# Kernel optimization log

Hardware: AMD Instinct MI355X
Metric: run time of the kernel (lower is better)

The kernel has to match this reference:

```python
import jax, jax.numpy as jnp
import numpy as np

N_NODES = 50000
N_EDGES = 640000
D = 128


def _sage_conv(x, src, dst, W_l, b, W_r, n_nodes):
    # PyG SAGEConv with mean aggregation:
    #   out = lin_l(mean_{j in N(i)} x_j) + lin_r(x_i)
    msg = x[src]                                              # [E, D] gather
    agg = jax.ops.segment_sum(msg, dst, num_segments=n_nodes)  # [N, D] scatter-add
    cnt = jax.ops.segment_sum(jnp.ones((src.shape[0], 1), x.dtype), dst,
                              num_segments=n_nodes)            # [N, 1]
    agg = agg / jnp.maximum(cnt, 1.0)                          # mean (0 if no neighbors)
    return agg @ W_l + b + x @ W_r


def setup_inputs() -> dict:
    key = jax.random.key(0)
    ks = jax.random.split(key, 8)
    s = 1.0 / np.sqrt(D)
    x = jax.random.normal(ks[0], (N_NODES, D), dtype=jnp.float32)
    edge_index = jax.random.randint(ks[1], (2, N_EDGES), 0, N_NODES, dtype=jnp.int64)
    return {
        "x": x,
        "edge_index": edge_index,
        "W_l1": jax.random.normal(ks[2], (D, D), dtype=jnp.float32) * s,
        "b1": jnp.zeros((D,), jnp.float32),
        "W_r1": jax.random.normal(ks[3], (D, D), dtype=jnp.float32) * s,
        "W_l2": jax.random.normal(ks[4], (D, D), dtype=jnp.float32) * s,
        "b2": jnp.zeros((D,), jnp.float32),
        "W_r2": jax.random.normal(ks[5], (D, D), dtype=jnp.float32) * s,
        "W_l3": jax.random.normal(ks[6], (D, D), dtype=jnp.float32) * s,
        "b3": jnp.zeros((D,), jnp.float32),
        "W_r3": jax.random.normal(ks[7], (D, D), dtype=jnp.float32) * s,
    }


def reference(x, edge_index, W_l1, b1, W_r1, W_l2, b2, W_r2, W_l3, b3, W_r3):
    src, dst = edge_index[0], edge_index[1]
    n = x.shape[0]
    h = jax.nn.relu(_sage_conv(x, src, dst, W_l1, b1, W_r1, n))
    h = jax.nn.relu(_sage_conv(h, src, dst, W_l2, b2, W_r2, n))
    h = _sage_conv(h, src, dst, W_l3, b3, W_r3, n)
    return h
```

## Files before the change

kernel.cpp:

```cpp
#include <hip/hip_runtime.h>


__global__ void k_hist(const int* __restrict__ dst, int* __restrict__ deg, int E)
{
    int i = blockIdx.x * blockDim.x + threadIdx.x;
    int stride = gridDim.x * blockDim.x;
    for (; i < E; i += stride)
        atomicAdd(&deg[dst[i]], 1);
}

__global__ __launch_bounds__(1024) void k_scan(const int* __restrict__ deg,
                                               int* __restrict__ rp,
                                               int* __restrict__ cur, int n)
{
    __shared__ int wsum[16];
    __shared__ int carry_s;
    int tid = threadIdx.x, lane = tid & 63, w = tid >> 6;
    if (tid == 0) carry_s = 0;
    __syncthreads();
    for (int base = 0; base < n; base += 4096) {
        int i = base + tid * 4;
        int4 v = make_int4(0, 0, 0, 0);
        if (i + 3 < n) v = *(const int4*)(deg + i);
        else {
            if (i     < n) v.x = deg[i];
            if (i + 1 < n) v.y = deg[i + 1];
            if (i + 2 < n) v.z = deg[i + 2];
            if (i + 3 < n) v.w = deg[i + 3];
        }
        int t = v.x + v.y + v.z + v.w;
        int s = t;
        #pragma unroll
        for (int d = 1; d < 64; d <<= 1) { int u = __shfl_up(s, d); if (lane >= d) s += u; }
        if (lane == 63) wsum[w] = s;
        __syncthreads();
        if (w == 0 && lane < 16) {
            int u = wsum[lane];
            #pragma unroll
            for (int d = 1; d < 16; d <<= 1) { int y = __shfl_up(u, d); if (lane >= d) u += y; }
            wsum[lane] = u;
        }
        __syncthreads();
        int carry = carry_s;
        int off = carry + (w ? wsum[w - 1] : 0) + (s - t);
        int r0 = off, r1 = r0 + v.x, r2 = r1 + v.y, r3 = r2 + v.z;
        if (i + 3 < n) {
            *(int4*)(rp + i)  = make_int4(r0, r1, r2, r3);
            *(int4*)(cur + i) = make_int4(r0, r1, r2, r3);
        } else {
            if (i     < n) { rp[i]     = r0; cur[i]     = r0; }
            if (i + 1 < n) { rp[i + 1] = r1; cur[i + 1] = r1; }
            if (i + 2 < n) { rp[i + 2] = r2; cur[i + 2] = r2; }
            if (i + 3 < n) { rp[i + 3] = r3; cur[i + 3] = r3; }
        }
        __syncthreads();
        if (tid == 1023) carry_s = carry + wsum[15];
    }
    __syncthreads();
    if (tid == 0) rp[n] = carry_s;
}

__global__ void k_fill(const int* __restrict__ src, const int* __restrict__ dst,
                       int* __restrict__ cur, int* __restrict__ col, int E)
{
    int i = blockIdx.x * blockDim.x + threadIdx.x;
    int stride = gridDim.x * blockDim.x;
    for (; i < E; i += stride) {
        int p = atomicAdd(&cur[dst[i]], 1);
        col[p] = src[i];
    }
}

__global__ __launch_bounds__(256) void k_agg(const float* __restrict__ h,
                                             const int* __restrict__ rp,
                                             const int* __restrict__ col,
                                             float* __restrict__ agg, int nNodes)
{
    int gw   = (blockIdx.x * blockDim.x + threadIdx.x) >> 6;
    int lane = threadIdx.x & 63;
    int nw   = (gridDim.x * blockDim.x) >> 6;
    for (int n = gw; n < nNodes; n += nw) {
        int s = rp[n], e = rp[n + 1];
        float a0 = 0.f, a1 = 0.f, b0 = 0.f, b1 = 0.f;
        int i = s;
        for (; i + 2 <= e; i += 2) {
            int c0 = col[i], c1 = col[i + 1];
            float2 v0 = *(const float2*)(h + (size_t)c0 * 128 + lane * 2);
            float2 v1 = *(const float2*)(h + (size_t)c1 * 128 + lane * 2);
            a0 += v0.x; a1 += v0.y;
            b0 += v1.x; b1 += v1.y;
        }
        if (i < e) {
            int c0 = col[i];
            float2 v0 = *(const float2*)(h + (size_t)c0 * 128 + lane * 2);
            a0 += v0.x; a1 += v0.y;
        }
        float inv = (e > s) ? (1.f / (float)(e - s)) : 0.f;
        float2 o; o.x = (a0 + b0) * inv; o.y = (a1 + b1) * inv;
        *(float2*)(agg + (size_t)n * 128 + lane * 2) = o;
    }
}

__global__ __launch_bounds__(256) void k_gemm(const float* __restrict__ agg,
                                              const float* hmat,
                                              const float* __restrict__ Wl,
                                              const float* __restrict__ Wr,
                                              const float* __restrict__ bias,
                                              float* out, int relu, int nNodes)
{
    __shared__ float Wc[64 * 128];
    __shared__ float inT[64 * 64];
    int tid = threadIdx.x;
    int node0 = blockIdx.x * 64;
    int ng = tid >> 4, cg = tid & 15;
    float acc[4][8];
    #pragma unroll
    for (int a = 0; a < 4; ++a)
        #pragma unroll
        for (int b = 0; b < 8; ++b) acc[a][b] = 0.f;

    int sn  = tid >> 2;
    int sk  = (tid & 3) * 16;
    int gsn = node0 + sn;

    #pragma unroll 1
    for (int ch = 0; ch < 4; ++ch) {
        const float* W  = (ch < 2) ? Wl : Wr;
        const float* in = (ch < 2) ? agg : hmat;
        int kc = (ch & 1) * 64;
        __syncthreads();
        {
            const float4* W4  = (const float4*)(W + kc * 128);
            float4* Wc4 = (float4*)Wc;
            #pragma unroll
            for (int it = 0; it < 8; ++it)
                Wc4[tid + it * 256] = W4[tid + it * 256];
        }
        if (gsn < nNodes) {
            const float4* s4 = (const float4*)(in + (size_t)gsn * 128 + kc + sk);
            #pragma unroll
            for (int j = 0; j < 4; ++j) {
                float4 v = s4[j];
                int k = sk + j * 4;
                inT[(k + 0) * 64 + sn] = v.x;
                inT[(k + 1) * 64 + sn] = v.y;
                inT[(k + 2) * 64 + sn] = v.z;
                inT[(k + 3) * 64 + sn] = v.w;
            }
        } else {
            #pragma unroll
            for (int j = 0; j < 4; ++j) {
                int k = sk + j * 4;
                inT[(k + 0) * 64 + sn] = 0.f;
                inT[(k + 1) * 64 + sn] = 0.f;
                inT[(k + 2) * 64 + sn] = 0.f;
                inT[(k + 3) * 64 + sn] = 0.f;
            }
        }
        __syncthreads();
        #pragma unroll 8
        for (int k = 0; k < 64; ++k) {
            float4 a4 = *(const float4*)(inT + k * 64 + ng * 4);
            float4 w0 = *(const float4*)(Wc + k * 128 + cg * 8);
            float4 w1 = *(const float4*)(Wc + k * 128 + cg * 8 + 4);
            float av[4] = {a4.x, a4.y, a4.z, a4.w};
            float wv[8] = {w0.x, w0.y, w0.z, w0.w, w1.x, w1.y, w1.z, w1.w};
            #pragma unroll
            for (int a = 0; a < 4; ++a)
                #pragma unroll
                for (int b = 0; b < 8; ++b)
                    acc[a][b] = fmaf(av[a], wv[b], acc[a][b]);
        }
    }
    float bv[8];
    #pragma unroll
    for (int b = 0; b < 8; ++b) bv[b] = bias[cg * 8 + b];
    #pragma unroll
    for (int a = 0; a < 4; ++a) {
        int gn = node0 + ng * 4 + a;
        if (gn >= nNodes) break;
        float r[8];
        #pragma unroll
        for (int b = 0; b < 8; ++b) {
            float v = acc[a][b] + bv[b];
            r[b] = relu ? fmaxf(v, 0.f) : v;
        }
        float4* o4 = (float4*)(out + (size_t)gn * 128 + cg * 8);
        o4[0] = *(float4*)(r);
        o4[1] = *(float4*)(r + 4);
    }
}

extern "C" void kernel_launch(void* const* d_in, const int* in_sizes, int n_in,
                              void* d_out, int out_size, void* d_ws, size_t ws_size,
                              hipStream_t stream)
{
    const float* x   = (const float*)d_in[0];
    const int*   ei  = (const int*)d_in[1];
    const float* Wl1 = (const float*)d_in[2];
    const float* b1  = (const float*)d_in[3];
    const float* Wr1 = (const float*)d_in[4];
    const float* Wl2 = (const float*)d_in[5];
    const float* b2  = (const float*)d_in[6];
    const float* Wr2 = (const float*)d_in[7];
    const float* Wl3 = (const float*)d_in[8];
    const float* b3  = (const float*)d_in[9];
    const float* Wr3 = (const float*)d_in[10];
    float* out = (float*)d_out;

    int N = in_sizes[0] / 128;
    int E = in_sizes[1] / 2;
    const int* srcp = ei;
    const int* dstp = ei + E;

    float* A  = (float*)d_ws;
    float* B  = A + (size_t)N * 128;
    int* deg  = (int*)(B + (size_t)N * 128);
    int* rp   = deg + ((N + 3) & ~3);
    int* cur  = rp + ((N + 4) & ~3);
    int* col  = cur + ((N + 3) & ~3);

    hipMemsetAsync(deg, 0, (size_t)N * sizeof(int), stream);
    k_hist<<<1024, 256, 0, stream>>>(dstp, deg, E);
    k_scan<<<1, 1024, 0, stream>>>(deg, rp, cur, N);
    k_fill<<<1024, 256, 0, stream>>>(srcp, dstp, cur, col, E);

    int gb = (N + 63) / 64;
    k_agg<<<2048, 256, 0, stream>>>(x, rp, col, A, N);
    k_gemm<<<gb, 256, 0, stream>>>(A, x, Wl1, Wr1, b1, B, 1, N);
    k_agg<<<2048, 256, 0, stream>>>(B, rp, col, A, N);
    k_gemm<<<gb, 256, 0, stream>>>(A, B, Wl2, Wr2, b2, B, 1, N);
    k_agg<<<2048, 256, 0, stream>>>(B, rp, col, A, N);
    k_gemm<<<gb, 256, 0, stream>>>(A, B, Wl3, Wr3, b3, out, 0, N);
}
```

Baseline: 493.5 us.

## Unroll gather loop by four and software-pipeline GEMM staging through registers

The aggregation loop now keeps four neighbor gathers in flight per iteration instead of two, and the aggregation grid doubles to 4096 blocks. The GEMM shrinks its K-chunk to 32 so shared memory drops, and it prefetches the next chunk of inputs and weights into registers while computing the current one. It also remaps threads so each wave covers a fixed column group. The aim is to hide global-memory latency in both kernels, at the cost of higher register pressure and more barriers per GEMM.

```diff
diff --git a/kernel.cpp b/kernel.cpp
--- a/kernel.cpp
+++ b/kernel.cpp
@@ -82,21 +82,28 @@
     for (int n = gw; n < nNodes; n += nw) {
         int s = rp[n], e = rp[n + 1];
         float a0 = 0.f, a1 = 0.f, b0 = 0.f, b1 = 0.f;
+        float c0 = 0.f, c1 = 0.f, d0 = 0.f, d1 = 0.f;
         int i = s;
-        for (; i + 2 <= e; i += 2) {
-            int c0 = col[i], c1 = col[i + 1];
-            float2 v0 = *(const float2*)(h + (size_t)c0 * 128 + lane * 2);
-            float2 v1 = *(const float2*)(h + (size_t)c1 * 128 + lane * 2);
+        for (; i + 4 <= e; i += 4) {
+            int e0 = col[i], e1 = col[i + 1], e2 = col[i + 2], e3 = col[i + 3];
+            float2 v0 = *(const float2*)(h + (size_t)e0 * 128 + lane * 2);
+            float2 v1 = *(const float2*)(h + (size_t)e1 * 128 + lane * 2);
+            float2 v2 = *(const float2*)(h + (size_t)e2 * 128 + lane * 2);
+            float2 v3 = *(const float2*)(h + (size_t)e3 * 128 + lane * 2);
             a0 += v0.x; a1 += v0.y;
             b0 += v1.x; b1 += v1.y;
-        }
-        if (i < e) {
-            int c0 = col[i];
-            float2 v0 = *(const float2*)(h + (size_t)c0 * 128 + lane * 2);
+            c0 += v2.x; c1 += v2.y;
+            d0 += v3.x; d1 += v3.y;
+        }
+        for (; i < e; ++i) {
+            int e0 = col[i];
+            float2 v0 = *(const float2*)(h + (size_t)e0 * 128 + lane * 2);
             a0 += v0.x; a1 += v0.y;
         }
         float inv = (e > s) ? (1.f / (float)(e - s)) : 0.f;
-        float2 o; o.x = (a0 + b0) * inv; o.y = (a1 + b1) * inv;
+        float2 o;
+        o.x = ((a0 + b0) + (c0 + d0)) * inv;
+        o.y = ((a1 + b1) + (c1 + d1)) * inv;
         *(float2*)(agg + (size_t)n * 128 + lane * 2) = o;
     }
 }
@@ -108,58 +115,63 @@
                                               const float* __restrict__ bias,
                                               float* out, int relu, int nNodes)
 {
-    __shared__ float Wc[64 * 128];
-    __shared__ float inT[64 * 64];
-    int tid = threadIdx.x;
-    int node0 = blockIdx.x * 64;
-    int ng = tid >> 4, cg = tid & 15;
+    __shared__ float inT[32 * 64];
+    __shared__ float Wc[32 * 128];
+    const int tid  = threadIdx.x;
+    const int wave = tid >> 6, l = tid & 63;
+    const int ng   = l & 15;
+    const int cg   = wave * 4 + (l >> 4);
+    const int node0 = blockIdx.x * 64;
+
+    const int sn  = tid >> 2;
+    const int skq = (tid & 3) * 8;
+    const int gsn = node0 + sn;
+
     float acc[4][8];
     #pragma unroll
     for (int a = 0; a < 4; ++a)
         #pragma unroll
         for (int b = 0; b < 8; ++b) acc[a][b] = 0.f;
 
-    int sn  = tid >> 2;
-    int sk  = (tid & 3) * 16;
-    int gsn = node0 + sn;
+    float rin[8];
+    float rw[16];
+
+    auto stage_load = [&](int ch) {
+        const float* src = (ch < 4) ? agg : hmat;
+        const int kc = (ch & 3) * 32;
+        const float* W = (ch < 4) ? (Wl + kc * 128) : (Wr + kc * 128);
+        if (gsn < nNodes) {
+            const float4* p = (const float4*)(src + (size_t)gsn * 128 + kc + skq);
+            *(float4*)(rin)     = p[0];
+            *(float4*)(rin + 4) = p[1];
+        } else {
+            #pragma unroll
+            for (int j = 0; j < 8; ++j) rin[j] = 0.f;
+        }
+        const float4* W4 = (const float4*)W;
+        #pragma unroll
+        for (int j = 0; j < 4; ++j)
+            *(float4*)(rw + j * 4) = W4[tid + j * 256];
+    };
+    auto stage_write = [&]() {
+        #pragma unroll
+        for (int j = 0; j < 8; ++j)
+            inT[(skq + j) * 64 + sn] = rin[j];
+        float4* Wc4 = (float4*)Wc;
+        #pragma unroll
+        for (int j = 0; j < 4; ++j)
+            Wc4[tid + j * 256] = *(float4*)(rw + j * 4);
+    };
+
+    stage_load(0);
+    stage_write();
+    __syncthreads();
 
     #pragma unroll 1
-    for (int ch = 0; ch < 4; ++ch) {
-        const float* W  = (ch < 2) ? Wl : Wr;
-        const float* in = (ch < 2) ? agg : hmat;
-        int kc = (ch & 1) * 64;
-        __syncthreads();
-        {
-            const float4* W4  = (const float4*)(W + kc * 128);
-            float4* Wc4 = (float4*)Wc;
-            #pragma unroll
-            for (int it = 0; it < 8; ++it)
-                Wc4[tid + it * 256] = W4[tid + it * 256];
-        }
-        if (gsn < nNodes) {
-            const float4* s4 = (const float4*)(in + (size_t)gsn * 128 + kc + sk);
-            #pragma unroll
-            for (int j = 0; j < 4; ++j) {
-                float4 v = s4[j];
-                int k = sk + j * 4;
-                inT[(k + 0) * 64 + sn] = v.x;
-                inT[(k + 1) * 64 + sn] = v.y;
-                inT[(k + 2) * 64 + sn] = v.z;
-                inT[(k + 3) * 64 + sn] = v.w;
-            }
-        } else {
-            #pragma unroll
-            for (int j = 0; j < 4; ++j) {
-                int k = sk + j * 4;
-                inT[(k + 0) * 64 + sn] = 0.f;
-                inT[(k + 1) * 64 + sn] = 0.f;
-                inT[(k + 2) * 64 + sn] = 0.f;
-                inT[(k + 3) * 64 + sn] = 0.f;
-            }
-        }
-        __syncthreads();
+    for (int ch = 0; ch < 8; ++ch) {
+        if (ch < 7) stage_load(ch + 1);
         #pragma unroll 8
-        for (int k = 0; k < 64; ++k) {
+        for (int k = 0; k < 32; ++k) {
             float4 a4 = *(const float4*)(inT + k * 64 + ng * 4);
             float4 w0 = *(const float4*)(Wc + k * 128 + cg * 8);
             float4 w1 = *(const float4*)(Wc + k * 128 + cg * 8 + 4);
@@ -171,23 +183,30 @@
                 for (int b = 0; b < 8; ++b)
                     acc[a][b] = fmaf(av[a], wv[b], acc[a][b]);
         }
-    }
+        __syncthreads();
+        if (ch < 7) {
+            stage_write();
+            __syncthreads();
+        }
+    }
+
     float bv[8];
     #pragma unroll
     for (int b = 0; b < 8; ++b) bv[b] = bias[cg * 8 + b];
     #pragma unroll
     for (int a = 0; a < 4; ++a) {
         int gn = node0 + ng * 4 + a;
-        if (gn >= nNodes) break;
-        float r[8];
-        #pragma unroll
-        for (int b = 0; b < 8; ++b) {
-            float v = acc[a][b] + bv[b];
-            r[b] = relu ? fmaxf(v, 0.f) : v;
-        }
-        float4* o4 = (float4*)(out + (size_t)gn * 128 + cg * 8);
-        o4[0] = *(float4*)(r);
-        o4[1] = *(float4*)(r + 4);
+        if (gn < nNodes) {
+            float r[8];
+            #pragma unroll
+            for (int b = 0; b < 8; ++b) {
+                float v = acc[a][b] + bv[b];
+                r[b] = relu ? fmaxf(v, 0.f) : v;
+            }
+            float4* o4 = (float4*)(out + (size_t)gn * 128 + cg * 8);
+            o4[0] = *(float4*)(r);
+            o4[1] = *(float4*)(r + 4);
+        }
     }
 }
 
@@ -226,10 +245,10 @@
     k_fill<<<1024, 256, 0, stream>>>(srcp, dstp, cur, col, E);
 
     int gb = (N + 63) / 64;
-    k_agg<<<2048, 256, 0, stream>>>(x, rp, col, A, N);
+    k_agg<<<4096, 256, 0, stream>>>(x, rp, col, A, N);
     k_gemm<<<gb, 256, 0, stream>>>(A, x, Wl1, Wr1, b1, B, 1, N);
-    k_agg<<<2048, 256, 0, stream>>>(B, rp, col, A, N);
+    k_agg<<<4096, 256, 0, stream>>>(B, rp, col, A, N);
     k_gemm<<<gb, 256, 0, stream>>>(A, B, Wl2, Wr2, b2, B, 1, N);
-    k_agg<<<2048, 256, 0, stream>>>(B, rp, col, A, N);
+    k_agg<<<4096, 256, 0, stream>>>(B, rp, col, A, N);
     k_gemm<<<gb, 256, 0, stream>>>(A, B, Wl3, Wr3, b3, out, 0, N);
 }
```

After: 502.6 us. No clear change (+1.9%).

## Use split-bf16 MFMA GEMM and hi/lo bf16 activations for aggregation

Applied to the files above, without the earlier changes.

Replaces the scalar fp32 FMA GEMM with MFMA 32x32x16 bf16 instructions. The bf16x3 split (hi*hi + hi*lo + lo*hi) keeps accuracy close to fp32. Activations are stored as separate hi and lo bf16 planes, and the weights are pre-split into a swizzled LDS image. The GEMM prefetches the next K chunk into registers while computing the current one. The goal is to cut GEMM compute time. The costs are three MFMAs per product, extra split kernels, and an aggregation that reads two planes, so its gather traffic stays the same with extra unpack ALU work.

```diff
diff --git a/kernel.cpp b/kernel.cpp
--- a/kernel.cpp
+++ b/kernel.cpp
@@ -1,12 +1,24 @@
 #include <hip/hip_runtime.h>
-
+#include <stdint.h>
+
+
+using bf16x8 = __attribute__((ext_vector_type(8))) __bf16;
+using f32x16 = __attribute__((ext_vector_type(16))) float;
+
+__device__ inline unsigned short f2bf(float v) {
+    uint32_t u = __float_as_uint(v);
+    uint32_t r = u + 0x7FFF + ((u >> 16) & 1);
+    return (unsigned short)(r >> 16);
+}
+__device__ inline float bf2f(unsigned short h) {
+    return __uint_as_float(((uint32_t)h) << 16);
+}
 
 __global__ void k_hist(const int* __restrict__ dst, int* __restrict__ deg, int E)
 {
     int i = blockIdx.x * blockDim.x + threadIdx.x;
     int stride = gridDim.x * blockDim.x;
-    for (; i < E; i += stride)
-        atomicAdd(&deg[dst[i]], 1);
+    for (; i < E; i += stride) atomicAdd(&deg[dst[i]], 1);
 }
 
 __global__ __launch_bounds__(1024) void k_scan(const int* __restrict__ deg,
@@ -71,10 +83,52 @@
     }
 }
 
-__global__ __launch_bounds__(256) void k_agg(const float* __restrict__ h,
-                                             const int* __restrict__ rp,
-                                             const int* __restrict__ col,
-                                             float* __restrict__ agg, int nNodes)
+__global__ __launch_bounds__(256) void k_splitX(const float* __restrict__ x,
+                                                unsigned short* __restrict__ ph,
+                                                unsigned short* __restrict__ pl,
+                                                int total4)
+{
+    int i = blockIdx.x * blockDim.x + threadIdx.x;
+    int stride = gridDim.x * blockDim.x;
+    for (; i < total4; i += stride) {
+        float4 v = ((const float4*)x)[i];
+        ushort4 h, l;
+        float f;
+        h.x = f2bf(v.x); f = bf2f(h.x); l.x = f2bf(v.x - f);
+        h.y = f2bf(v.y); f = bf2f(h.y); l.y = f2bf(v.y - f);
+        h.z = f2bf(v.z); f = bf2f(h.z); l.z = f2bf(v.z - f);
+        h.w = f2bf(v.w); f = bf2f(h.w); l.w = f2bf(v.w - f);
+        ((ushort4*)ph)[i] = h;
+        ((ushort4*)pl)[i] = l;
+    }
+}
+
+__global__ __launch_bounds__(256) void k_splitW(const float* __restrict__ Wl,
+                                                const float* __restrict__ Wr,
+                                                unsigned short* __restrict__ img)
+{
+    int idx = blockIdx.x * 256 + threadIdx.x;
+    int ch = idx >> 13;
+    int rem = idx & 8191;
+    int kk = rem >> 7;
+    int c  = rem & 127;
+    int kg = (ch & 1) * 64 + kk;
+    float v = (ch < 2 ? Wl : Wr)[kg * 128 + c];
+    unsigned short h = f2bf(v);
+    unsigned short l = f2bf(v - bf2f(h));
+    int sl = (kk >> 3) ^ (c & 7);
+    int o  = ch * 16384 + c * 64 + sl * 8 + (kk & 7);
+    img[o]        = h;
+    img[o + 8192] = l;
+}
+
+__global__ __launch_bounds__(256) void k_aggP(const unsigned short* __restrict__ hh,
+                                              const unsigned short* __restrict__ hl,
+                                              const int* __restrict__ rp,
+                                              const int* __restrict__ col,
+                                              unsigned short* __restrict__ ah,
+                                              unsigned short* __restrict__ al,
+                                              int nNodes)
 {
     int gw   = (blockIdx.x * blockDim.x + threadIdx.x) >> 6;
     int lane = threadIdx.x & 63;
@@ -85,109 +139,142 @@
         int i = s;
         for (; i + 2 <= e; i += 2) {
             int c0 = col[i], c1 = col[i + 1];
-            float2 v0 = *(const float2*)(h + (size_t)c0 * 128 + lane * 2);
-            float2 v1 = *(const float2*)(h + (size_t)c1 * 128 + lane * 2);
-            a0 += v0.x; a1 += v0.y;
-            b0 += v1.x; b1 += v1.y;
+            uint32_t h0 = *(const uint32_t*)(hh + (size_t)c0 * 128 + lane * 2);
+            uint32_t l0 = *(const uint32_t*)(hl + (size_t)c0 * 128 + lane * 2);
+            uint32_t h1 = *(const uint32_t*)(hh + (size_t)c1 * 128 + lane * 2);
+            uint32_t l1 = *(const uint32_t*)(hl + (size_t)c1 * 128 + lane * 2);
+            a0 += __uint_as_float(h0 << 16) + __uint_as_float(l0 << 16);
+            a1 += __uint_as_float(h0 & 0xffff0000u) + __uint_as_float(l0 & 0xffff0000u);
+            b0 += __uint_as_float(h1 << 16) + __uint_as_float(l1 << 16);
+            b1 += __uint_as_float(h1 & 0xffff0000u) + __uint_as_float(l1 & 0xffff0000u);
         }
         if (i < e) {
             int c0 = col[i];
-            float2 v0 = *(const float2*)(h + (size_t)c0 * 128 + lane * 2);
-            a0 += v0.x; a1 += v0.y;
+            uint32_t h0 = *(const uint32_t*)(hh + (size_t)c0 * 128 + lane * 2);
+            uint32_t l0 = *(const uint32_t*)(hl + (size_t)c0 * 128 + lane * 2);
+            a0 += __uint_as_float(h0 << 16) + __uint_as_float(l0 << 16);
+            a1 += __uint_as_float(h0 & 0xffff0000u) + __uint_as_float(l0 & 0xffff0000u);
         }
         float inv = (e > s) ? (1.f / (float)(e - s)) : 0.f;
-        float2 o; o.x = (a0 + b0) * inv; o.y = (a1 + b1) * inv;
-        *(float2*)(agg + (size_t)n * 128 + lane * 2) = o;
-    }
-}
-
-__global__ __launch_bounds__(256) void k_gemm(const float* __restrict__ agg,
-                                              const float* hmat,
-                                              const float* __restrict__ Wl,
-                                              const float* __restrict__ Wr,
+        float m0 = (a0 + b0) * inv, m1 = (a1 + b1) * inv;
+        unsigned short h0s = f2bf(m0), h1s = f2bf(m1);
+        unsigned short l0s = f2bf(m0 - bf2f(h0s)), l1s = f2bf(m1 - bf2f(h1s));
+        *(uint32_t*)(ah + (size_t)n * 128 + lane * 2) = (uint32_t)h0s | ((uint32_t)h1s << 16);
+        *(uint32_t*)(al + (size_t)n * 128 + lane * 2) = (uint32_t)l0s | ((uint32_t)l1s << 16);
+    }
+}
+
+__global__ __launch_bounds__(256) void k_gemm(const unsigned short* __restrict__ aggH,
+                                              const unsigned short* __restrict__ aggL,
+                                              const unsigned short* hH,
+                                              const unsigned short* hL,
+                                              const unsigned short* __restrict__ wimg,
                                               const float* __restrict__ bias,
-                                              float* out, int relu, int nNodes)
-{
-    __shared__ float Wc[64 * 128];
-    __shared__ float inT[64 * 64];
-    int tid = threadIdx.x;
-    int node0 = blockIdx.x * 64;
-    int ng = tid >> 4, cg = tid & 15;
-    float acc[4][8];
+                                              float* outF,
+                                              unsigned short* oH,
+                                              unsigned short* oL,
+                                              int relu, int nNodes)
+{
+    __shared__ unsigned short lds[24576];
+    constexpr int AH = 0, AL = 4096, BH = 8192, BL = 16384;
+
+    const int tid  = threadIdx.x;
+    const int wave = tid >> 6, l = tid & 63;
+    const int lh   = l >> 5, l31 = l & 31;
+    const int wm = wave >> 1, wn = wave & 1;
+    const int m0w = wm * 32, n0w = wn * 64;
+    const int node0 = blockIdx.x * 64;
+
+    const int r_s   = tid >> 3;
+    const int sp    = tid & 7;
+    const int ssrc  = sp ^ (r_s & 7);
+    const int offA  = r_s * 64 + sp * 8;
+
+    f32x16 acc0, acc1;
     #pragma unroll
-    for (int a = 0; a < 4; ++a)
+    for (int i = 0; i < 16; ++i) { acc0[i] = 0.f; acc1[i] = 0.f; }
+
+    uint4 rA[4];
+    uint4 rB[8];
+
+    auto load12 = [&](int ch) {
+        const unsigned short* sH = (ch < 2) ? aggH : hH;
+        const unsigned short* sL = (ch < 2) ? aggL : hL;
+        const int k0 = (ch & 1) * 64;
+        size_t r0 = (size_t)min(node0 + r_s,      nNodes - 1) * 128 + k0 + ssrc * 8;
+        size_t r1 = (size_t)min(node0 + 32 + r_s, nNodes - 1) * 128 + k0 + ssrc * 8;
+        rA[0] = *(const uint4*)(sH + r0);
+        rA[1] = *(const uint4*)(sH + r1);
+        rA[2] = *(const uint4*)(sL + r0);
+        rA[3] = *(const uint4*)(sL + r1);
+        const unsigned short* w = wimg + ch * 16384;
         #pragma unroll
-        for (int b = 0; b < 8; ++b) acc[a][b] = 0.f;
-
-    int sn  = tid >> 2;
-    int sk  = (tid & 3) * 16;
-    int gsn = node0 + sn;
-
+        for (int s = 0; s < 4; ++s) {
+            rB[s]     = *(const uint4*)(w + s * 2048 + tid * 8);
+            rB[4 + s] = *(const uint4*)(w + 8192 + s * 2048 + tid * 8);
+        }
+    };
+    auto write12 = [&]() {
+        *(uint4*)&lds[AH + offA]        = rA[0];
+        *(uint4*)&lds[AH + 2048 + offA] = rA[1];
+        *(uint4*)&lds[AL + offA]        = rA[2];
+        *(uint4*)&lds[AL + 2048 + offA] = rA[3];
+        #pragma unroll
+        for (int s = 0; s < 4; ++s) {
+            *(uint4*)&lds[BH + s * 2048 + tid * 8] = rB[s];
+            *(uint4*)&lds[BL + s * 2048 + tid * 8] = rB[4 + s];
+        }
+    };
+
+    load12(0);
     #pragma unroll 1
     for (int ch = 0; ch < 4; ++ch) {
-        const float* W  = (ch < 2) ? Wl : Wr;
-        const float* in = (ch < 2) ? agg : hmat;
-        int kc = (ch & 1) * 64;
-        __syncthreads();
-        {
-            const float4* W4  = (const float4*)(W + kc * 128);
-            float4* Wc4 = (float4*)Wc;
-            #pragma unroll
-            for (int it = 0; it < 8; ++it)
-                Wc4[tid + it * 256] = W4[tid + it * 256];
-        }
-        if (gsn < nNodes) {
-            const float4* s4 = (const float4*)(in + (size_t)gsn * 128 + kc + sk);
-            #pragma unroll
-            for (int j = 0; j < 4; ++j) {
-                float4 v = s4[j];
-                int k = sk + j * 4;
-                inT[(k + 0) * 64 + sn] = v.x;
-                inT[(k + 1) * 64 + sn] = v.y;
-                inT[(k + 2) * 64 + sn] = v.z;
-                inT[(k + 3) * 64 + sn] = v.w;
+        __syncthreads();
+        write12();
+        __syncthreads();
+        if (ch < 3) load12(ch + 1);
+
+        const int rowA = m0w + l31;
+        const int rowB0 = n0w + l31, rowB1 = rowB0 + 32;
+        #pragma unroll
+        for (int ks = 0; ks < 4; ++ks) {
+            const int sg = ks * 2 + lh;
+            bf16x8 a_h = *(const bf16x8*)&lds[AH + rowA * 64 + ((sg ^ (rowA & 7)) << 3)];
+            bf16x8 a_l = *(const bf16x8*)&lds[AL + rowA * 64 + ((sg ^ (rowA & 7)) << 3)];
+            bf16x8 b_h0 = *(const bf16x8*)&lds[BH + rowB0 * 64 + ((sg ^ (rowB0 & 7)) << 3)];
+            bf16x8 b_l0 = *(const bf16x8*)&lds[BL + rowB0 * 64 + ((sg ^ (rowB0 & 7)) << 3)];
+            bf16x8 b_h1 = *(const bf16x8*)&lds[BH + rowB1 * 64 + ((sg ^ (rowB1 & 7)) << 3)];
+            bf16x8 b_l1 = *(const bf16x8*)&lds[BL + rowB1 * 64 + ((sg ^ (rowB1 & 7)) << 3)];
+            acc0 = __builtin_amdgcn_mfma_f32_32x32x16_bf16(a_h, b_h0, acc0, 0, 0, 0);
+            acc1 = __builtin_amdgcn_mfma_f32_32x32x16_bf16(a_h, b_h1, acc1, 0, 0, 0);
+            acc0 = __builtin_amdgcn_mfma_f32_32x32x16_bf16(a_h, b_l0, acc0, 0, 0, 0);
+            acc1 = __builtin_amdgcn_mfma_f32_32x32x16_bf16(a_h, b_l1, acc1, 0, 0, 0);
+            acc0 = __builtin_amdgcn_mfma_f32_32x32x16_bf16(a_l, b_h0, acc0, 0, 0, 0);
+            acc1 = __builtin_amdgcn_mfma_f32_32x32x16_bf16(a_l, b_h1, acc1, 0, 0, 0);
+        }
+    }
+
+    const float bv0 = bias[n0w + l31];
+    const float bv1 = bias[n0w + 32 + l31];
+    #pragma unroll
+    for (int reg = 0; reg < 16; ++reg) {
+        int row = (reg & 3) + 8 * (reg >> 2) + 4 * lh;
+        int gn  = node0 + m0w + row;
+        if (gn < nNodes) {
+            float v0 = acc0[reg] + bv0;
+            float v1 = acc1[reg] + bv1;
+            if (relu) { v0 = fmaxf(v0, 0.f); v1 = fmaxf(v1, 0.f); }
+            if (outF) {
+                outF[(size_t)gn * 128 + n0w + l31]      = v0;
+                outF[(size_t)gn * 128 + n0w + 32 + l31] = v1;
+            } else {
+                unsigned short h0 = f2bf(v0), h1 = f2bf(v1);
+                oH[(size_t)gn * 128 + n0w + l31]      = h0;
+                oH[(size_t)gn * 128 + n0w + 32 + l31] = h1;
+                oL[(size_t)gn * 128 + n0w + l31]      = f2bf(v0 - bf2f(h0));
+                oL[(size_t)gn * 128 + n0w + 32 + l31] = f2bf(v1 - bf2f(h1));
             }
-        } else {
-            #pragma unroll
-            for (int j = 0; j < 4; ++j) {
-                int k = sk + j * 4;
-                inT[(k + 0) * 64 + sn] = 0.f;
-                inT[(k + 1) * 64 + sn] = 0.f;
-                inT[(k + 2) * 64 + sn] = 0.f;
-                inT[(k + 3) * 64 + sn] = 0.f;
-            }
-        }
-        __syncthreads();
-        #pragma unroll 8
-        for (int k = 0; k < 64; ++k) {
-            float4 a4 = *(const float4*)(inT + k * 64 + ng * 4);
-            float4 w0 = *(const float4*)(Wc + k * 128 + cg * 8);
-            float4 w1 = *(const float4*)(Wc + k * 128 + cg * 8 + 4);
-            float av[4] = {a4.x, a4.y, a4.z, a4.w};
-            float wv[8] = {w0.x, w0.y, w0.z, w0.w, w1.x, w1.y, w1.z, w1.w};
-            #pragma unroll
-            for (int a = 0; a < 4; ++a)
-                #pragma unroll
-                for (int b = 0; b < 8; ++b)
-                    acc[a][b] = fmaf(av[a], wv[b], acc[a][b]);
-        }
-    }
-    float bv[8];
-    #pragma unroll
-    for (int b = 0; b < 8; ++b) bv[b] = bias[cg * 8 + b];
-    #pragma unroll
-    for (int a = 0; a < 4; ++a) {
-        int gn = node0 + ng * 4 + a;
-        if (gn >= nNodes) break;
-        float r[8];
-        #pragma unroll
-        for (int b = 0; b < 8; ++b) {
-            float v = acc[a][b] + bv[b];
-            r[b] = relu ? fmaxf(v, 0.f) : v;
-        }
-        float4* o4 = (float4*)(out + (size_t)gn * 128 + cg * 8);
-        o4[0] = *(float4*)(r);
-        o4[1] = *(float4*)(r + 4);
+        }
     }
 }
 
@@ -206,30 +293,45 @@
     const float* Wl3 = (const float*)d_in[8];
     const float* b3  = (const float*)d_in[9];
     const float* Wr3 = (const float*)d_in[10];
-    float* out = (float*)d_out;
 
     int N = in_sizes[0] / 128;
     int E = in_sizes[1] / 2;
     const int* srcp = ei;
     const int* dstp = ei + E;
-
-    float* A  = (float*)d_ws;
-    float* B  = A + (size_t)N * 128;
-    int* deg  = (int*)(B + (size_t)N * 128);
-    int* rp   = deg + ((N + 3) & ~3);
-    int* cur  = rp + ((N + 4) & ~3);
-    int* col  = cur + ((N + 3) & ~3);
+    size_t P = (size_t)N * 128;
+
+    unsigned short* Xh = (unsigned short*)d_ws;
+    unsigned short* Xl = Xh + P;
+    unsigned short* Ah = Xl + P;
+    unsigned short* Al = Ah + P;
+    int* deg = (int*)(Al + P);
+    int* rp  = deg + ((N + 3) & ~3);
+    int* cur = rp + ((N + 4) & ~3);
+    int* col = cur + ((N + 3) & ~3);
+    unsigned short* Wimg = (unsigned short*)(col + ((E + 3) & ~3));
+
+    unsigned short* Oh = (unsigned short*)d_out;
+    unsigned short* Ol = Oh + P;
+    float* out = (float*)d_out;
 
     hipMemsetAsync(deg, 0, (size_t)N * sizeof(int), stream);
     k_hist<<<1024, 256, 0, stream>>>(dstp, deg, E);
     k_scan<<<1, 1024, 0, stream>>>(deg, rp, cur, N);
     k_fill<<<1024, 256, 0, stream>>>(srcp, dstp, cur, col, E);
 
+    k_splitX<<<512, 256, 0, stream>>>(x, Xh, Xl, (int)(P / 4));
+    k_splitW<<<128, 256, 0, stream>>>(Wl1, Wr1, Wimg);
+    k_splitW<<<128, 256, 0, stream>>>(Wl2, Wr2, Wimg + 65536);
+    k_splitW<<<128, 256, 0, stream>>>(Wl3, Wr3, Wimg + 131072);
+
     int gb = (N + 63) / 64;
-    k_agg<<<2048, 256, 0, stream>>>(x, rp, col, A, N);
-    k_gemm<<<gb, 256, 0, stream>>>(A, x, Wl1, Wr1, b1, B, 1, N);
-    k_agg<<<2048, 256, 0, stream>>>(B, rp, col, A, N);
-    k_gemm<<<gb, 256, 0, stream>>>(A, B, Wl2, Wr2, b2, B, 1, N);
-    k_agg<<<2048, 256, 0, stream>>>(B, rp, col, A, N);
-    k_gemm<<<gb, 256, 0, stream>>>(A, B, Wl3, Wr3, b3, out, 0, N);
-}
+    k_aggP<<<4096, 256, 0, stream>>>(Xh, Xl, rp, col, Ah, Al, N);
+    k_gemm<<<gb, 256, 0, stream>>>(Ah, Al, Xh, Xl, Wimg, b1,
+                                   nullptr, Oh, Ol, 1, N);
+    k_aggP<<<4096, 256, 0, stream>>>(Oh, Ol, rp, col, Ah, Al, N);
+    k_gemm<<<gb, 256, 0, stream>>>(Ah, Al, Oh, Ol, Wimg + 65536, b2,
+                                   nullptr, Xh, Xl, 1, N);
+    k_aggP<<<4096, 256, 0, stream>>>(Xh, Xl, rp, col, Ah, Al, N);
+    k_gemm<<<gb, 256, 0, stream>>>(Ah, Al, Xh, Xl, Wimg + 131072, b3,
+                                   out, nullptr, nullptr, 0, N);
+}
```

New measurement: 540.2 us. 1.09x slower.
